# Optimization experiments

Measured on AMD Instinct MI355X. Metric: run time of the kernel, lower is better.

The kernel has to match this reference:

```python
import jax, jax.numpy as jnp
import numpy as np

B, C, H, W = 2, 128, 96, 96
HEADS, DHEAD, WIN = 4, 32, 5
INNER = HEADS * DHEAD
PAD = WIN // 2


def setup_inputs() -> dict:
    key = jax.random.key(0)
    k1, k2, k3, k4, k5 = jax.random.split(key, 5)
    s = 1.0 / np.sqrt(C)
    return {
        "x": jax.random.normal(k1, (B, C, H, W), dtype=jnp.float32),
        "wq": jax.random.normal(k2, (INNER, C), dtype=jnp.float32) * s,
        "wk": jax.random.normal(k3, (INNER, C), dtype=jnp.float32) * s,
        "wv": jax.random.normal(k4, (INNER, C), dtype=jnp.float32) * s,
        "wproj": jax.random.normal(k5, (C, INNER), dtype=jnp.float32) * s,
    }


def _windows(t):
    # same neighborhood ordering as F.unfold (row-major over kernel offsets).
    tp = jnp.pad(t, ((0, 0), (0, 0), (0, 0), (PAD, PAD), (PAD, PAD)))
    wins = [tp[:, :, :, di:di + H, dj:dj + W]
            for di in range(WIN) for dj in range(WIN)]
    return jnp.stack(wins, axis=3)


def reference(x, wq, wk, wv, wproj):
    # 1x1 convs == per-pixel linear maps
    q = jnp.einsum('oc,bcxy->boxy', wq, x).reshape(B, HEADS, DHEAD, H, W)
    k = jnp.einsum('oc,bcxy->boxy', wk, x).reshape(B, HEADS, DHEAD, H, W)
    v = jnp.einsum('oc,bcxy->boxy', wv, x).reshape(B, HEADS, DHEAD, H, W)

    k_win = _windows(k)  # (B,h,d,25,H,W)
    v_win = _windows(v)

    scale = 1.0 / np.sqrt(DHEAD)
    attn = jnp.einsum('bhdxy,bhdkxy->bhkxy', q, k_win) * scale
    attn = jax.nn.softmax(attn, axis=2)  # softmax over the 25 window positions
    out = jnp.einsum('bhkxy,bhdkxy->bhdxy', attn, v_win)

    out = out.reshape(B, INNER, H, W)
    return jnp.einsum('co,boxy->bcxy', wproj, out)
```

## Files before the change

kernel.cpp:

```cpp
#include <hip/hip_runtime.h>
#include <hip/hip_bf16.h>
#include <hip/hip_fp16.h>

#define PP 9216
#define OO 384

typedef _Float16 f16x8 __attribute__((ext_vector_type(8)));
typedef _Float16 h2    __attribute__((ext_vector_type(2)));
typedef float    f32x4 __attribute__((ext_vector_type(4)));

#if defined(__has_builtin)
# if __has_builtin(__builtin_amdgcn_fdot2)
#  define HAS_FDOT2 1
# endif
#endif

__device__ __forceinline__ float dot2acc(h2 a, h2 b, float c) {
#ifdef HAS_FDOT2
    return __builtin_amdgcn_fdot2(a, b, c, false);
#else
    return c + (float)a[0] * (float)b[0] + (float)a[1] * (float)b[1];
#endif
}

__global__ __launch_bounds__(256) void prep(
    const float* __restrict__ x, const float* __restrict__ wq,
    const float* __restrict__ wk, const float* __restrict__ wv,
    _Float16* __restrict__ xT, _Float16* __restrict__ wqkv)
{
    const int t = threadIdx.x;
    if (blockIdx.y == 4) {
        if (blockIdx.z) return;
        int idx = blockIdx.x * 256 + t;
        if (idx < 49152) {
            int o = idx >> 7;
            const float* src = (o < 128) ? wq : ((o < 256) ? wk : wv);
            wqkv[idx] = (_Float16)src[(o & 127) * 128 + (idx & 127)];
        }
        return;
    }
    __shared__ float sT[32][33];
    const int p0 = blockIdx.x * 32;
    const int c0 = blockIdx.y * 32;
    const int b  = blockIdx.z;
    const int row = t >> 3, col = t & 7;

    const float* xb = x + (size_t)b * 128 * PP;
    float4 v = *(const float4*)(xb + (size_t)(c0 + row) * PP + p0 + col * 4);
    sT[col * 4 + 0][row] = v.x;
    sT[col * 4 + 1][row] = v.y;
    sT[col * 4 + 2][row] = v.z;
    sT[col * 4 + 3][row] = v.w;
    __syncthreads();

    _Float16 h[4];
    #pragma unroll
    for (int j = 0; j < 4; j++) h[j] = (_Float16)sT[row][col * 4 + j];
    *(ushort4*)(xT + (size_t)b * PP * 128 + (size_t)(p0 + row) * 128 + c0 + col * 4) =
        *(ushort4*)h;
}

__global__ __launch_bounds__(256) void qkv_gemm(
    const _Float16* __restrict__ xT, const _Float16* __restrict__ wqkv,
    _Float16* __restrict__ qkv)
{
    __shared__ _Float16 sEpi[4][32][104];

    const int b = blockIdx.z;
    const int p0 = blockIdx.x * 64;
    const int nbase = blockIdx.y * 192;
    const int t = threadIdx.x;
    const int w = t >> 6, lane = t & 63;
    const int lm = lane & 15, quad = lane >> 4;
    const int ms0 = (w & 1) * 32;
    const int nw = (w >> 1) * 96;

    const _Float16* xb = xT + (size_t)b * PP * 128;
    _Float16* qb = qkv + (size_t)b * PP * OO;

    f16x8 A[2][4];
    #pragma unroll
    for (int ms = 0; ms < 2; ms++)
        #pragma unroll
        for (int kc = 0; kc < 4; kc++)
            A[ms][kc] = *(const f16x8*)(xb + (size_t)(p0 + ms0 + ms * 16 + lm) * 128
                                        + kc * 32 + quad * 8);

    for (int nt = 0; nt < 6; nt++) {
        const int n0 = nbase + nw + nt * 16;
        f16x8 Bf[4];
        #pragma unroll
        for (int kc = 0; kc < 4; kc++)
            Bf[kc] = *(const f16x8*)(wqkv + (size_t)(n0 + lm) * 128 + kc * 32 + quad * 8);
        f32x4 acc[2];
        #pragma unroll
        for (int ms = 0; ms < 2; ms++) {
            acc[ms] = (f32x4){0.f, 0.f, 0.f, 0.f};
            #pragma unroll
            for (int kc = 0; kc < 4; kc++)
                acc[ms] = __builtin_amdgcn_mfma_f32_16x16x32_f16(A[ms][kc], Bf[kc], acc[ms], 0, 0, 0);
        }
        #pragma unroll
        for (int ms = 0; ms < 2; ms++)
            #pragma unroll
            for (int r = 0; r < 4; r++)
                sEpi[w][ms * 16 + quad * 4 + r][nt * 16 + lm] = (_Float16)acc[ms][r];
    }

    #pragma unroll
    for (int it = 0; it < 6; it++) {
        int idx = it * 64 + lane;
        int row = idx / 12;
        int ch  = idx % 12;
        uint4 v = *(const uint4*)&sEpi[w][row][ch * 8];
        *(uint4*)(qb + (size_t)(p0 + ms0 + row) * OO + nbase + nw + ch * 8) = v;
    }
}

__global__ __launch_bounds__(256) void attn_proj(
    const _Float16* __restrict__ qkv, const float* __restrict__ wp,
    float* __restrict__ out)
{
    __shared__ _Float16 sK[96 * 40];
    __shared__ _Float16 sV[96 * 40];
    __shared__ float    sS[32 * 29];
    __shared__ _Float16 sAo[32 * 136];

    const int t  = threadIdx.x;
    const int x0 = blockIdx.x * 8;
    const int y0 = blockIdx.y * 4;
    const int b  = blockIdx.z;
    const _Float16* base = qkv + (size_t)b * PP * OO;

    const int px = t & 31, w8 = t >> 5;
    const int ly = px >> 3, lx = px & 7;
    const int gp0 = (y0 + ly) * 96 + x0 + lx;
    const float scale = 0.17677669529663689f;

    for (int h = 0; h < 4; h++) {
        if (t < 192) {
            const int arr = (t >= 96) ? 1 : 0;
            const int pos = t - 96 * arr;
            const int gy = y0 - 2 + pos / 12;
            const int gx = x0 - 2 + pos % 12;
            _Float16* dst = (arr ? sV : sK) + pos * 40;
            if ((unsigned)gy < 96u && (unsigned)gx < 96u) {
                const _Float16* src = base + (size_t)(gy * 96 + gx) * OO + 128 + arr * 128 + h * 32;
                #pragma unroll
                for (int j = 0; j < 4; j++)
                    *(uint4*)(dst + j * 8) = *(const uint4*)(src + j * 8);
            } else {
                uint4 z = {0u, 0u, 0u, 0u};
                #pragma unroll
                for (int j = 0; j < 4; j++) *(uint4*)(dst + j * 8) = z;
            }
        }
        h2 qreg[16];
        {
            const _Float16* qs = base + (size_t)gp0 * OO + h * 32;
            #pragma unroll
            for (int j = 0; j < 4; j++)
                *(uint4*)(&qreg[j * 4]) = *(const uint4*)(qs + j * 8);
        }
        __syncthreads();

        for (int pos = w8; pos < 25; pos += 8) {
            const int hp = (ly + pos / 5) * 12 + lx + pos % 5;
            const _Float16* kr = sK + hp * 40;
            h2 kreg[16];
            #pragma unroll
            for (int j = 0; j < 4; j++)
                *(uint4*)(&kreg[j * 4]) = *(const uint4*)(kr + j * 8);
            float s0 = 0.f, s1 = 0.f;
            #pragma unroll
            for (int j = 0; j < 8; j++) {
                s0 = dot2acc(qreg[2 * j], kreg[2 * j], s0);
                s1 = dot2acc(qreg[2 * j + 1], kreg[2 * j + 1], s1);
            }
            sS[px * 29 + pos] = (s0 + s1) * scale;
        }
        __syncthreads();

        if (t < 32) {
            float* row = sS + t * 29;
            float m = row[0];
            #pragma unroll
            for (int p = 1; p < 25; p++) m = fmaxf(m, row[p]);
            float sum = 0.f;
            float e[25];
            #pragma unroll
            for (int p = 0; p < 25; p++) { e[p] = __expf(row[p] - m); sum += e[p]; }
            const float inv = 1.f / sum;
            #pragma unroll
            for (int p = 0; p < 25; p++) row[p] = e[p] * inv;
        }
        __syncthreads();

        float at[25];
        #pragma unroll
        for (int p = 0; p < 25; p++) at[p] = sS[px * 29 + p];

        float f[4] = {0.f, 0.f, 0.f, 0.f};
        for (int p = 0; p < 25; p++) {
            const int hp = (ly + p / 5) * 12 + lx + p % 5;
            h2 vreg[2];
            *(uint2*)vreg = *(const uint2*)(sV + hp * 40 + w8 * 4);
            #pragma unroll
            for (int j = 0; j < 2; j++) {
                f[2 * j]     += at[p] * (float)vreg[j][0];
                f[2 * j + 1] += at[p] * (float)vreg[j][1];
            }
        }
        _Float16 ho[4];
        #pragma unroll
        for (int j = 0; j < 4; j++) ho[j] = (_Float16)f[j];
        *(ushort4*)(sAo + px * 136 + h * 32 + w8 * 4) = *(ushort4*)ho;
        __syncthreads();
    }

    const int lane = t & 63, w4 = t >> 6;
    const int lm = lane & 15, quad = lane >> 4;

    f16x8 Aw[2][4];
    #pragma unroll
    for (int mt = 0; mt < 2; mt++)
        #pragma unroll
        for (int kc = 0; kc < 4; kc++) {
            const float* ws_ = wp + (size_t)(w4 * 32 + mt * 16 + lm) * 128 + kc * 32 + quad * 8;
            float4 a0 = *(const float4*)ws_;
            float4 a1 = *(const float4*)(ws_ + 4);
            Aw[mt][kc] = (f16x8){(_Float16)a0.x, (_Float16)a0.y, (_Float16)a0.z, (_Float16)a0.w,
                                 (_Float16)a1.x, (_Float16)a1.y, (_Float16)a1.z, (_Float16)a1.w};
        }

    f32x4 acc[2][2];
    #pragma unroll
    for (int mt = 0; mt < 2; mt++)
        #pragma unroll
        for (int nt = 0; nt < 2; nt++)
            acc[mt][nt] = (f32x4){0.f, 0.f, 0.f, 0.f};

    #pragma unroll
    for (int nt = 0; nt < 2; nt++) {
        f16x8 Bf[4];
        #pragma unroll
        for (int kc = 0; kc < 4; kc++)
            Bf[kc] = *(const f16x8*)(sAo + (nt * 16 + lm) * 136 + kc * 32 + quad * 8);
        #pragma unroll
        for (int mt = 0; mt < 2; mt++)
            #pragma unroll
            for (int kc = 0; kc < 4; kc++)
                acc[mt][nt] = __builtin_amdgcn_mfma_f32_16x16x32_f16(Aw[mt][kc], Bf[kc], acc[mt][nt], 0, 0, 0);
    }

    float* ob = out + (size_t)b * 128 * PP;
    #pragma unroll
    for (int mt = 0; mt < 2; mt++)
        #pragma unroll
        for (int nt = 0; nt < 2; nt++) {
            const int pxl = nt * 16 + lm;
            const int gpl = (y0 + (pxl >> 3)) * 96 + x0 + (pxl & 7);
            #pragma unroll
            for (int r = 0; r < 4; r++) {
                const int c = w4 * 32 + mt * 16 + quad * 4 + r;
                ob[(size_t)c * PP + gpl] = acc[mt][nt][r];
            }
        }
}

extern "C" void kernel_launch(void* const* d_in, const int* in_sizes, int n_in,
                              void* d_out, int out_size, void* d_ws, size_t ws_size,
                              hipStream_t stream)
{
    const float* x  = (const float*)d_in[0];
    const float* wq = (const float*)d_in[1];
    const float* wk = (const float*)d_in[2];
    const float* wv = (const float*)d_in[3];
    const float* wp = (const float*)d_in[4];
    float* out = (float*)d_out;

    _Float16* ws    = (_Float16*)d_ws;
    _Float16* xT    = ws;
    _Float16* wqkv  = xT + 2359296;
    _Float16* qkvh  = wqkv + 49152;

    prep<<<dim3(288, 5, 2), 256, 0, stream>>>(x, wq, wk, wv, xT, wqkv);
    qkv_gemm<<<dim3(144, 2, 2), 256, 0, stream>>>(xT, wqkv, qkvh);
    attn_proj<<<dim3(12, 24, 2), 256, 0, stream>>>(qkvh, wp, out);
}
```

Measured before the change: 110.8 us.

## Fuse transpose/cast prep into QKV GEMM and process all heads at once in attention

Removes the separate prep kernel: the QKV GEMM now loads fp32 x tiles into shared memory, transposes and converts to fp16 while building MFMA fragments, and converts the fp32 weights on the fly. The attention kernel loads the K and V halos for all four heads in one pass and computes scores, softmax and the weighted sum for all heads together, which removes the per-head loop and its many barriers. This trades an extra launch and an intermediate global round-trip for more shared memory and registers per block, and lower occupancy is a possible cost.

```diff
diff --git a/kernel.cpp b/kernel.cpp
--- a/kernel.cpp
+++ b/kernel.cpp
@@ -23,48 +23,12 @@
 #endif
 }
 
-__global__ __launch_bounds__(256) void prep(
+__global__ __launch_bounds__(256) void qkv_fused(
     const float* __restrict__ x, const float* __restrict__ wq,
     const float* __restrict__ wk, const float* __restrict__ wv,
-    _Float16* __restrict__ xT, _Float16* __restrict__ wqkv)
-{
-    const int t = threadIdx.x;
-    if (blockIdx.y == 4) {
-        if (blockIdx.z) return;
-        int idx = blockIdx.x * 256 + t;
-        if (idx < 49152) {
-            int o = idx >> 7;
-            const float* src = (o < 128) ? wq : ((o < 256) ? wk : wv);
-            wqkv[idx] = (_Float16)src[(o & 127) * 128 + (idx & 127)];
-        }
-        return;
-    }
-    __shared__ float sT[32][33];
-    const int p0 = blockIdx.x * 32;
-    const int c0 = blockIdx.y * 32;
-    const int b  = blockIdx.z;
-    const int row = t >> 3, col = t & 7;
-
-    const float* xb = x + (size_t)b * 128 * PP;
-    float4 v = *(const float4*)(xb + (size_t)(c0 + row) * PP + p0 + col * 4);
-    sT[col * 4 + 0][row] = v.x;
-    sT[col * 4 + 1][row] = v.y;
-    sT[col * 4 + 2][row] = v.z;
-    sT[col * 4 + 3][row] = v.w;
-    __syncthreads();
-
-    _Float16 h[4];
-    #pragma unroll
-    for (int j = 0; j < 4; j++) h[j] = (_Float16)sT[row][col * 4 + j];
-    *(ushort4*)(xT + (size_t)b * PP * 128 + (size_t)(p0 + row) * 128 + c0 + col * 4) =
-        *(ushort4*)h;
-}
-
-__global__ __launch_bounds__(256) void qkv_gemm(
-    const _Float16* __restrict__ xT, const _Float16* __restrict__ wqkv,
     _Float16* __restrict__ qkv)
 {
-    __shared__ _Float16 sEpi[4][32][104];
+    __shared__ float sX[128][68];
 
     const int b = blockIdx.z;
     const int p0 = blockIdx.x * 64;
@@ -75,44 +39,73 @@
     const int ms0 = (w & 1) * 32;
     const int nw = (w >> 1) * 96;
 
-    const _Float16* xb = xT + (size_t)b * PP * 128;
+    const float* xb = x + (size_t)b * 128 * PP;
     _Float16* qb = qkv + (size_t)b * PP * OO;
 
+    #pragma unroll
+    for (int i = 0; i < 8; i++) {
+        int idx = t + 256 * i;
+        int c  = idx >> 4;
+        int p4 = idx & 15;
+        *(float4*)&sX[c][p4 * 4] = *(const float4*)(xb + (size_t)c * PP + p0 + p4 * 4);
+    }
+    __syncthreads();
+
     f16x8 A[2][4];
     #pragma unroll
-    for (int ms = 0; ms < 2; ms++)
-        #pragma unroll
-        for (int kc = 0; kc < 4; kc++)
-            A[ms][kc] = *(const f16x8*)(xb + (size_t)(p0 + ms0 + ms * 16 + lm) * 128
-                                        + kc * 32 + quad * 8);
-
+    for (int ms = 0; ms < 2; ms++) {
+        const int px = ms0 + ms * 16 + lm;
+        #pragma unroll
+        for (int kc = 0; kc < 4; kc++) {
+            const int c0 = kc * 32 + quad * 8;
+            f16x8 a;
+            #pragma unroll
+            for (int j = 0; j < 8; j++) a[j] = (_Float16)sX[c0 + j][px];
+            A[ms][kc] = a;
+        }
+    }
+
+    f32x4 acc[6][2];
+    #pragma unroll
     for (int nt = 0; nt < 6; nt++) {
-        const int n0 = nbase + nw + nt * 16;
+        const int o0 = nbase + nw + nt * 16 + lm;
+        const float* wsrc = (o0 < 128) ? (wq + (size_t)o0 * 128)
+                          : (o0 < 256) ? (wk + (size_t)(o0 - 128) * 128)
+                                       : (wv + (size_t)(o0 - 256) * 128);
         f16x8 Bf[4];
         #pragma unroll
-        for (int kc = 0; kc < 4; kc++)
-            Bf[kc] = *(const f16x8*)(wqkv + (size_t)(n0 + lm) * 128 + kc * 32 + quad * 8);
-        f32x4 acc[2];
+        for (int kc = 0; kc < 4; kc++) {
+            float4 a0 = *(const float4*)(wsrc + kc * 32 + quad * 8);
+            float4 a1 = *(const float4*)(wsrc + kc * 32 + quad * 8 + 4);
+            Bf[kc] = (f16x8){(_Float16)a0.x, (_Float16)a0.y, (_Float16)a0.z, (_Float16)a0.w,
+                             (_Float16)a1.x, (_Float16)a1.y, (_Float16)a1.z, (_Float16)a1.w};
+        }
         #pragma unroll
         for (int ms = 0; ms < 2; ms++) {
-            acc[ms] = (f32x4){0.f, 0.f, 0.f, 0.f};
+            acc[nt][ms] = (f32x4){0.f, 0.f, 0.f, 0.f};
             #pragma unroll
             for (int kc = 0; kc < 4; kc++)
-                acc[ms] = __builtin_amdgcn_mfma_f32_16x16x32_f16(A[ms][kc], Bf[kc], acc[ms], 0, 0, 0);
-        }
+                acc[nt][ms] = __builtin_amdgcn_mfma_f32_16x16x32_f16(A[ms][kc], Bf[kc], acc[nt][ms], 0, 0, 0);
+        }
+    }
+
+    __syncthreads();
+
+    _Float16* sE = (_Float16*)&sX[0][0] + w * (32 * 104);
+    #pragma unroll
+    for (int nt = 0; nt < 6; nt++)
         #pragma unroll
         for (int ms = 0; ms < 2; ms++)
             #pragma unroll
             for (int r = 0; r < 4; r++)
-                sEpi[w][ms * 16 + quad * 4 + r][nt * 16 + lm] = (_Float16)acc[ms][r];
-    }
+                sE[(ms * 16 + quad * 4 + r) * 104 + nt * 16 + lm] = (_Float16)acc[nt][ms][r];
 
     #pragma unroll
     for (int it = 0; it < 6; it++) {
         int idx = it * 64 + lane;
         int row = idx / 12;
         int ch  = idx % 12;
-        uint4 v = *(const uint4*)&sEpi[w][row][ch * 8];
+        uint4 v = *(const uint4*)(sE + row * 104 + ch * 8);
         *(uint4*)(qb + (size_t)(p0 + ms0 + row) * OO + nbase + nw + ch * 8) = v;
     }
 }
@@ -121,9 +114,8 @@
     const _Float16* __restrict__ qkv, const float* __restrict__ wp,
     float* __restrict__ out)
 {
-    __shared__ _Float16 sK[96 * 40];
-    __shared__ _Float16 sV[96 * 40];
-    __shared__ float    sS[32 * 29];
+    __shared__ _Float16 sKV[96 * 264];
+    __shared__ float    sS[128 * 26];
     __shared__ _Float16 sAo[32 * 136];
 
     const int t  = threadIdx.x;
@@ -132,41 +124,39 @@
     const int b  = blockIdx.z;
     const _Float16* base = qkv + (size_t)b * PP * OO;
 
-    const int px = t & 31, w8 = t >> 5;
+    #pragma unroll
+    for (int i = 0; i < 12; i++) {
+        int idx = t + 256 * i;
+        int pos = idx >> 5;
+        int ch  = idx & 31;
+        int gy = y0 - 2 + pos / 12;
+        int gx = x0 - 2 + pos % 12;
+        uint4 v = {0u, 0u, 0u, 0u};
+        if ((unsigned)gy < 96u && (unsigned)gx < 96u)
+            v = *(const uint4*)(base + (size_t)(gy * 96 + gx) * OO + 128 + ch * 8);
+        *(uint4*)(sKV + pos * 264 + ch * 8) = v;
+    }
+
+    const int px = t & 31, h = (t >> 5) & 3, pg = t >> 7;
     const int ly = px >> 3, lx = px & 7;
     const int gp0 = (y0 + ly) * 96 + x0 + lx;
+    const int r = h * 32 + px;
     const float scale = 0.17677669529663689f;
 
-    for (int h = 0; h < 4; h++) {
-        if (t < 192) {
-            const int arr = (t >= 96) ? 1 : 0;
-            const int pos = t - 96 * arr;
-            const int gy = y0 - 2 + pos / 12;
-            const int gx = x0 - 2 + pos % 12;
-            _Float16* dst = (arr ? sV : sK) + pos * 40;
-            if ((unsigned)gy < 96u && (unsigned)gx < 96u) {
-                const _Float16* src = base + (size_t)(gy * 96 + gx) * OO + 128 + arr * 128 + h * 32;
-                #pragma unroll
-                for (int j = 0; j < 4; j++)
-                    *(uint4*)(dst + j * 8) = *(const uint4*)(src + j * 8);
-            } else {
-                uint4 z = {0u, 0u, 0u, 0u};
-                #pragma unroll
-                for (int j = 0; j < 4; j++) *(uint4*)(dst + j * 8) = z;
-            }
-        }
-        h2 qreg[16];
-        {
-            const _Float16* qs = base + (size_t)gp0 * OO + h * 32;
-            #pragma unroll
-            for (int j = 0; j < 4; j++)
-                *(uint4*)(&qreg[j * 4]) = *(const uint4*)(qs + j * 8);
-        }
-        __syncthreads();
-
-        for (int pos = w8; pos < 25; pos += 8) {
+    h2 qreg[16];
+    {
+        const _Float16* qs = base + (size_t)gp0 * OO + h * 32;
+        #pragma unroll
+        for (int j = 0; j < 4; j++)
+            *(uint4*)(&qreg[j * 4]) = *(const uint4*)(qs + j * 8);
+    }
+    __syncthreads();
+
+    {
+        const int pbeg = pg ? 13 : 0, pend = pg ? 25 : 13;
+        for (int pos = pbeg; pos < pend; pos++) {
             const int hp = (ly + pos / 5) * 12 + lx + pos % 5;
-            const _Float16* kr = sK + hp * 40;
+            const _Float16* kr = sKV + hp * 264 + h * 32;
             h2 kreg[16];
             #pragma unroll
             for (int j = 0; j < 4; j++)
@@ -177,46 +167,53 @@
                 s0 = dot2acc(qreg[2 * j], kreg[2 * j], s0);
                 s1 = dot2acc(qreg[2 * j + 1], kreg[2 * j + 1], s1);
             }
-            sS[px * 29 + pos] = (s0 + s1) * scale;
-        }
-        __syncthreads();
-
-        if (t < 32) {
-            float* row = sS + t * 29;
-            float m = row[0];
-            #pragma unroll
-            for (int p = 1; p < 25; p++) m = fmaxf(m, row[p]);
-            float sum = 0.f;
-            float e[25];
-            #pragma unroll
-            for (int p = 0; p < 25; p++) { e[p] = __expf(row[p] - m); sum += e[p]; }
-            const float inv = 1.f / sum;
-            #pragma unroll
-            for (int p = 0; p < 25; p++) row[p] = e[p] * inv;
-        }
-        __syncthreads();
-
+            sS[r * 26 + pos] = (s0 + s1) * scale;
+        }
+    }
+    __syncthreads();
+
+    if (t < 128) {
+        float* row = sS + t * 26;
+        float m = row[0];
+        #pragma unroll
+        for (int p = 1; p < 25; p++) m = fmaxf(m, row[p]);
+        float sum = 0.f;
+        float e[25];
+        #pragma unroll
+        for (int p = 0; p < 25; p++) { e[p] = __expf(row[p] - m); sum += e[p]; }
+        const float inv = 1.f / sum;
+        #pragma unroll
+        for (int p = 0; p < 25; p++) row[p] = e[p] * inv;
+    }
+    __syncthreads();
+
+    {
         float at[25];
         #pragma unroll
-        for (int p = 0; p < 25; p++) at[p] = sS[px * 29 + p];
-
-        float f[4] = {0.f, 0.f, 0.f, 0.f};
+        for (int p = 0; p < 25; p++) at[p] = sS[r * 26 + p];
+
+        float f[16];
+        #pragma unroll
+        for (int j = 0; j < 16; j++) f[j] = 0.f;
         for (int p = 0; p < 25; p++) {
             const int hp = (ly + p / 5) * 12 + lx + p % 5;
-            h2 vreg[2];
-            *(uint2*)vreg = *(const uint2*)(sV + hp * 40 + w8 * 4);
-            #pragma unroll
-            for (int j = 0; j < 2; j++) {
+            const _Float16* vr = sKV + hp * 264 + 128 + h * 32 + pg * 16;
+            h2 vreg[8];
+            *(uint4*)(&vreg[0]) = *(const uint4*)vr;
+            *(uint4*)(&vreg[4]) = *(const uint4*)(vr + 8);
+            #pragma unroll
+            for (int j = 0; j < 8; j++) {
                 f[2 * j]     += at[p] * (float)vreg[j][0];
                 f[2 * j + 1] += at[p] * (float)vreg[j][1];
             }
         }
-        _Float16 ho[4];
-        #pragma unroll
-        for (int j = 0; j < 4; j++) ho[j] = (_Float16)f[j];
-        *(ushort4*)(sAo + px * 136 + h * 32 + w8 * 4) = *(ushort4*)ho;
-        __syncthreads();
-    }
+        _Float16 ho[16];
+        #pragma unroll
+        for (int j = 0; j < 16; j++) ho[j] = (_Float16)f[j];
+        *(uint4*)(sAo + px * 136 + h * 32 + pg * 16)     = *(uint4*)(&ho[0]);
+        *(uint4*)(sAo + px * 136 + h * 32 + pg * 16 + 8) = *(uint4*)(&ho[8]);
+    }
+    __syncthreads();
 
     const int lane = t & 63, w4 = t >> 6;
     const int lm = lane & 15, quad = lane >> 4;
@@ -261,9 +258,9 @@
             const int pxl = nt * 16 + lm;
             const int gpl = (y0 + (pxl >> 3)) * 96 + x0 + (pxl & 7);
             #pragma unroll
-            for (int r = 0; r < 4; r++) {
-                const int c = w4 * 32 + mt * 16 + quad * 4 + r;
-                ob[(size_t)c * PP + gpl] = acc[mt][nt][r];
+            for (int rr = 0; rr < 4; rr++) {
+                const int c = w4 * 32 + mt * 16 + quad * 4 + rr;
+                ob[(size_t)c * PP + gpl] = acc[mt][nt][rr];
             }
         }
 }
@@ -279,12 +276,8 @@
     const float* wp = (const float*)d_in[4];
     float* out = (float*)d_out;
 
-    _Float16* ws    = (_Float16*)d_ws;
-    _Float16* xT    = ws;
-    _Float16* wqkv  = xT + 2359296;
-    _Float16* qkvh  = wqkv + 49152;
-
-    prep<<<dim3(288, 5, 2), 256, 0, stream>>>(x, wq, wk, wv, xT, wqkv);
-    qkv_gemm<<<dim3(144, 2, 2), 256, 0, stream>>>(xT, wqkv, qkvh);
+    _Float16* qkvh = (_Float16*)d_ws;
+
+    qkv_fused<<<dim3(144, 2, 2), 256, 0, stream>>>(x, wq, wk, wv, qkvh);
     attn_proj<<<dim3(12, 24, 2), 256, 0, stream>>>(qkvh, wp, out);
 }
```

New measurement: 115.9 us. +4.6%, slower.
